# Kernel tuning notes

Hardware: AMD Instinct MI355X
Metric: run time of the kernel (lower is better)

Reference implementation:

```python
import math
import jax, jax.numpy as jnp
import numpy as np

N_TOTAL = 262144   # total objects across all groups
B = 4096           # number of groups (segments)
H = 256            # hidden_size
OS = 128           # object_size
CS = 256           # context_size


def setup_inputs() -> dict:
    key = jax.random.key(0)
    ks = jax.random.split(key, 12)
    s = 0.02
    return {
        "objects": jax.random.normal(ks[0], (N_TOTAL, OS), dtype=jnp.float32),
        "context": jax.random.normal(ks[1], (B, CS), dtype=jnp.float32),
        "segment_ids": jnp.sort(jax.random.randint(ks[2], (N_TOTAL,), 0, B, dtype=jnp.int32)),
        "num_segments": B,
        "W0": jax.random.normal(ks[3], (OS, H), dtype=jnp.float32) * s,
        "b0": jnp.zeros((H,), dtype=jnp.float32),
        "W1": jax.random.normal(ks[4], (H, H), dtype=jnp.float32) * s,
        "b1": jnp.zeros((H,), dtype=jnp.float32),
        "Wkv": jax.random.normal(ks[5], (H, 2 * H), dtype=jnp.float32) * s,
        "bkv": jnp.zeros((2 * H,), dtype=jnp.float32),
        "Wq": jax.random.normal(ks[6], (CS, H), dtype=jnp.float32) * s,
        "bq": jnp.zeros((H,), dtype=jnp.float32),
    }


def reference(objects, context, segment_ids, num_segments,
              W0, b0, W1, b1, Wkv, bkv, Wq, bq):
    # MLP over flattened objects: relu(fc0) -> relu(fc1)
    x = jax.nn.relu(objects @ W0 + b0)          # [N, H]
    x = jax.nn.relu(x @ W1 + b1)                # [N, H]
    kv = x @ Wkv + bkv                          # [N, 2H]
    k, v = kv[:, :H], kv[:, H:]                 # [N, H] each
    q = context @ Wq + bq                       # [B, H]
    q_per_obj = q[segment_ids]                  # repeat_interleave(query, split_sections)
    scale = 1.0 / math.sqrt(H)
    logits = jnp.einsum('of,of->o', q_per_obj, k) * scale  # [N]
    # per-segment stable softmax
    m = jax.ops.segment_max(logits, segment_ids, num_segments=num_segments)  # [B]
    e = jnp.exp(logits - m[segment_ids])                                     # [N]
    denom = jax.ops.segment_sum(e, segment_ids, num_segments=num_segments)   # [B]
    w = e / jnp.maximum(denom, 1e-9)[segment_ids]                            # [N]
    # per-segment weighted sum of values
    embedding = jax.ops.segment_sum(w[:, None] * v, segment_ids,
                                    num_segments=num_segments)               # [B, H]
    return embedding, w
```

## Files before the change

### kernel.cpp

```cpp
#include <hip/hip_runtime.h>
#include <hip/hip_bf16.h>


typedef __attribute__((ext_vector_type(8))) short bf16x8;
typedef __attribute__((ext_vector_type(4))) float f32x4;
typedef __attribute__((ext_vector_type(4))) short s16x4;

__device__ __forceinline__ float b2f(short s) {
    unsigned int u = ((unsigned int)(unsigned short)s) << 16;
    float f;
    __builtin_memcpy(&f, &u, 4);
    return f;
}
__device__ __forceinline__ short f2b(float x) {
    __hip_bfloat16 h = __float2bfloat16(x);
    short s;
    __builtin_memcpy(&s, &h, 2);
    return s;
}
__device__ __forceinline__ unsigned pack2(float a, float b) {
    return ((unsigned)(unsigned short)f2b(a)) | (((unsigned)(unsigned short)f2b(b)) << 16);
}
__device__ __forceinline__ f32x4 vmax0(f32x4 v) {
    f32x4 r;
    r[0] = fmaxf(v[0], 0.f); r[1] = fmaxf(v[1], 0.f);
    r[2] = fmaxf(v[2], 0.f); r[3] = fmaxf(v[3], 0.f);
    return r;
}

#define MFMA16(a, b, c) __builtin_amdgcn_mfma_f32_16x16x32_bf16(a, b, c, 0, 0, 0)
#define SWZ(row) (((row) & 7) << 4)

__global__ void kPrep0(const float* __restrict__ W0, const float* __restrict__ W1,
                       const float* __restrict__ Wkv, const float* __restrict__ Wq,
                       short* __restrict__ W0f, short* __restrict__ W1f,
                       short* __restrict__ Wkvb, short* __restrict__ Wqt) {
    int i = blockIdx.x * 256 + threadIdx.x;
    if (i < 32768) {
        int e = i & 7, lane = (i >> 3) & 63, ks = (i >> 9) & 3, mh = (i >> 11) & 3, wv = (i >> 13) & 3;
        int h = wv * 64 + mh * 16 + (lane & 15);
        int k = ks * 32 + (lane >> 4) * 8 + e;
        W0f[i] = f2b(W0[k * 256 + h]);
    }
    if (i < 65536) {
        int e = i & 7, lane = (i >> 3) & 63, ks = (i >> 9) & 7, mh = (i >> 12) & 3, wv = (i >> 14) & 3;
        int h = wv * 64 + mh * 16 + (lane & 15);
        int k = ks * 32 + (lane >> 4) * 8 + e;
        W1f[i] = f2b(W1[k * 256 + h]);
        int n = i >> 8, kk = i & 255;
        Wqt[i] = f2b(Wq[kk * 256 + n]);
    }
    if (i < 131072) Wkvb[i] = f2b(Wkv[i]);
}

__global__ __launch_bounds__(256) void kPrep1(
        const float* __restrict__ context, const short* __restrict__ Wqt,
        const float* __restrict__ bq, const short* __restrict__ Wkvb,
        const float* __restrict__ bkv, float* __restrict__ u_ws,
        float* __restrict__ c_ws) {
    __shared__ short cbuf[64 * 256];
    __shared__ float pl[4][64];
    const int t = threadIdx.x, w = t >> 6, l = t & 63;
    const int lo = l & 15, hi = l >> 4;
    const int base = blockIdx.x * 64;

    const float* src = context + (size_t)base * 256;
#pragma unroll
    for (int i = 0; i < 16; ++i) {
        int fi = (t + i * 256) * 4;
        float4 v = *(const float4*)(src + fi);
        int row = fi >> 8, col = fi & 255;
        int byte = (row << 9) + (col << 1);
        byte ^= SWZ(row);
        s16x4 pk;
        pk[0] = f2b(v.x); pk[1] = f2b(v.y); pk[2] = f2b(v.z); pk[3] = f2b(v.w);
        *(s16x4*)((char*)cbuf + byte) = pk;
    }
    __syncthreads();

    f32x4 acc[4][4] = {};
    const short* wqb = Wqt + (size_t)(w * 64 + lo) * 256 + hi * 8;
#pragma unroll
    for (int ks = 0; ks < 8; ++ks) {
        bf16x8 a[4], b[4];
#pragma unroll
        for (int m = 0; m < 4; ++m) {
            int row = m * 16 + lo;
            int byte = (row << 9) + ks * 64 + hi * 16;
            byte ^= SWZ(row);
            a[m] = *(const bf16x8*)((const char*)cbuf + byte);
        }
#pragma unroll
        for (int n = 0; n < 4; ++n) b[n] = *(const bf16x8*)(wqb + n * 16 * 256 + ks * 32);
#pragma unroll
        for (int m = 0; m < 4; ++m)
#pragma unroll
            for (int n = 0; n < 4; ++n) acc[m][n] = MFMA16(a[m], b[n], acc[m][n]);
    }
    __syncthreads();

    float bqv[4];
#pragma unroll
    for (int n = 0; n < 4; ++n) bqv[n] = bq[w * 64 + n * 16 + lo];
#pragma unroll
    for (int m = 0; m < 4; ++m)
#pragma unroll
        for (int n = 0; n < 4; ++n)
#pragma unroll
            for (int j = 0; j < 4; ++j) {
                float q = acc[m][n][j] + bqv[n];
                int row = m * 16 + hi * 4 + j;
                int col = w * 64 + n * 16 + lo;
                int byte = (row << 9) + (col << 1);
                byte ^= SWZ(row);
                *(short*)((char*)cbuf + byte) = f2b(q);
            }
    __syncthreads();

    {
        float p = 0.f;
#pragma unroll
        for (int j = 0; j < 8; ++j) {
            int col = w * 64 + j * 8;
            int byte = (l << 9) + (col << 1);
            byte ^= SWZ(l);
            bf16x8 xv = *(const bf16x8*)((const char*)cbuf + byte);
            const float* bp = bkv + col;
            p += b2f(xv[0]) * bp[0] + b2f(xv[1]) * bp[1] + b2f(xv[2]) * bp[2] + b2f(xv[3]) * bp[3]
               + b2f(xv[4]) * bp[4] + b2f(xv[5]) * bp[5] + b2f(xv[6]) * bp[6] + b2f(xv[7]) * bp[7];
        }
        pl[w][l] = p;
    }
    __syncthreads();
    if (t < 64) c_ws[base + t] = (pl[0][t] + pl[1][t] + pl[2][t] + pl[3][t]) * 0.0625f;

#pragma unroll
    for (int m = 0; m < 4; ++m)
#pragma unroll
        for (int n = 0; n < 4; ++n) acc[m][n] = (f32x4){0.f, 0.f, 0.f, 0.f};
    const short* wkb = Wkvb + (size_t)(w * 64 + lo) * 512 + hi * 8;
#pragma unroll
    for (int ks = 0; ks < 8; ++ks) {
        bf16x8 a[4], b[4];
#pragma unroll
        for (int m = 0; m < 4; ++m) {
            int row = m * 16 + lo;
            int byte = (row << 9) + ks * 64 + hi * 16;
            byte ^= SWZ(row);
            a[m] = *(const bf16x8*)((const char*)cbuf + byte);
        }
#pragma unroll
        for (int n = 0; n < 4; ++n) b[n] = *(const bf16x8*)(wkb + n * 16 * 512 + ks * 32);
#pragma unroll
        for (int m = 0; m < 4; ++m)
#pragma unroll
            for (int n = 0; n < 4; ++n) acc[m][n] = MFMA16(a[m], b[n], acc[m][n]);
    }
#pragma unroll
    for (int m = 0; m < 4; ++m)
#pragma unroll
        for (int n = 0; n < 4; ++n)
#pragma unroll
            for (int j = 0; j < 4; ++j) {
                int s = base + m * 16 + hi * 4 + j;
                int col = w * 64 + n * 16 + lo;
                u_ws[(size_t)s * 256 + col] = acc[m][n][j] * 0.0625f;
            }
}

__global__ __launch_bounds__(256, 3) void kA(
        const float* __restrict__ objects, const int* __restrict__ segids,
        const short* __restrict__ W0f, const short* __restrict__ W1f,
        const float* __restrict__ b0, const float* __restrict__ b1,
        const float* __restrict__ u_ws, const float* __restrict__ c_ws,
        float* __restrict__ e_ws, float* __restrict__ Y, float* __restrict__ D) {
    __shared__ char smem[49152];
    __shared__ float pl[4][64];
    __shared__ float e_sh[64];
    __shared__ int sid_sh[64];
    char* bufIn = smem;
    char* x1b   = smem + 16384;
    char* x2b   = smem;

    const int t = threadIdx.x, w = t >> 6, l = t & 63;
    const int lo = l & 15, hi = l >> 4;
    const int bid = (blockIdx.x & 7) * (gridDim.x >> 3) + (blockIdx.x >> 3);
    const size_t base_row = (size_t)bid * 64;

    if (t < 64) sid_sh[t] = segids[base_row + t];

    bf16x8 w0frag[4][4];
#pragma unroll
    for (int mh = 0; mh < 4; ++mh)
#pragma unroll
        for (int ks = 0; ks < 4; ++ks)
            w0frag[mh][ks] = *(const bf16x8*)(W0f + ((((w * 4 + mh) * 4 + ks) << 9) + (l << 3)));

    const float* src = objects + base_row * 128;
#pragma unroll
    for (int i = 0; i < 8; ++i) {
        int fi = (t + i * 256) * 4;
        float4 v = *(const float4*)(src + fi);
        int row = fi >> 7, col = fi & 127;
        int byte = (row << 8) + (col << 1);
        byte ^= SWZ(row);
        uint2 pk;
        pk.x = pack2(v.x, v.y);
        pk.y = pack2(v.z, v.w);
        *(uint2*)(bufIn + byte) = pk;
    }
    __syncthreads();

    f32x4 acc[4][4] = {};
#pragma unroll
    for (int ks = 0; ks < 4; ++ks) {
        bf16x8 bv[4];
#pragma unroll
        for (int nn = 0; nn < 4; ++nn) {
            int m = nn * 16 + lo;
            int byte = (m << 8) + (ks << 6) + (hi << 4);
            byte ^= SWZ(m);
            bv[nn] = *(const bf16x8*)(bufIn + byte);
        }
        __builtin_amdgcn_s_setprio(1);
#pragma unroll
        for (int mh = 0; mh < 4; ++mh)
#pragma unroll
            for (int nn = 0; nn < 4; ++nn) acc[mh][nn] = MFMA16(w0frag[mh][ks], bv[nn], acc[mh][nn]);
        __builtin_amdgcn_s_setprio(0);
    }

#pragma unroll
    for (int mh = 0; mh < 4; ++mh) {
        f32x4 bb = *(const f32x4*)(b0 + w * 64 + mh * 16 + hi * 4);
#pragma unroll
        for (int nn = 0; nn < 4; ++nn) {
            f32x4 v = vmax0(acc[mh][nn] + bb);
            int m = nn * 16 + lo;
            int byte = (m << 9) + ((w * 64 + mh * 16 + hi * 4) << 1);
            byte ^= SWZ(m);
            uint2 pk;
            pk.x = pack2(v[0], v[1]);
            pk.y = pack2(v[2], v[3]);
            *(uint2*)(x1b + byte) = pk;
        }
    }
    __syncthreads();

#pragma unroll
    for (int mh = 0; mh < 4; ++mh)
#pragma unroll
        for (int nn = 0; nn < 4; ++nn) acc[mh][nn] = (f32x4){0.f, 0.f, 0.f, 0.f};
#pragma unroll
    for (int ks = 0; ks < 8; ++ks) {
        bf16x8 av[4], bv[4];
#pragma unroll
        for (int mh = 0; mh < 4; ++mh)
            av[mh] = *(const bf16x8*)(W1f + ((((w * 4 + mh) * 8 + ks) << 9) + (l << 3)));
#pragma unroll
        for (int nn = 0; nn < 4; ++nn) {
            int m = nn * 16 + lo;
            int byte = (m << 9) + (ks << 6) + (hi << 4);
            byte ^= SWZ(m);
            bv[nn] = *(const bf16x8*)(x1b + byte);
        }
        __builtin_amdgcn_s_setprio(1);
#pragma unroll
        for (int mh = 0; mh < 4; ++mh)
#pragma unroll
            for (int nn = 0; nn < 4; ++nn) acc[mh][nn] = MFMA16(av[mh], bv[nn], acc[mh][nn]);
        __builtin_amdgcn_s_setprio(0);
    }

    int sids[4];
#pragma unroll
    for (int nn = 0; nn < 4; ++nn) sids[nn] = sid_sh[nn * 16 + lo];
    f32x4 pacc[4] = {};
#pragma unroll
    for (int mh = 0; mh < 4; ++mh) {
        f32x4 bb = *(const f32x4*)(b1 + w * 64 + mh * 16 + hi * 4);
#pragma unroll
        for (int nn = 0; nn < 4; ++nn) {
            f32x4 u4 = *(const f32x4*)(u_ws + (size_t)sids[nn] * 256 + w * 64 + mh * 16 + hi * 4);
            f32x4 v = vmax0(acc[mh][nn] + bb);
            acc[mh][nn] = v;
            pacc[nn] += v * u4;
        }
    }
#pragma unroll
    for (int nn = 0; nn < 4; ++nn) {
        float p = (pacc[nn][0] + pacc[nn][1]) + (pacc[nn][2] + pacc[nn][3]);
        p += __shfl_xor(p, 16);
        p += __shfl_xor(p, 32);
        if (hi == 0) pl[w][nn * 16 + lo] = p;
    }
    __syncthreads();

    if (t < 64) {
        float logit = pl[0][t] + pl[1][t] + pl[2][t] + pl[3][t] + c_ws[sid_sh[t]];
        float e = __expf(logit);
        e_sh[t] = e;
        e_ws[base_row + t] = e;
    }

#pragma unroll
    for (int mh = 0; mh < 4; ++mh) {
#pragma unroll
        for (int nn = 0; nn < 4; ++nn) {
            int m = nn * 16 + lo;
            int byte = (m << 9) + ((w * 64 + mh * 16 + hi * 4) << 1);
            byte ^= SWZ(m);
            uint2 pk;
            pk.x = pack2(acc[mh][nn][0], acc[mh][nn][1]);
            pk.y = pack2(acc[mh][nn][2], acc[mh][nn][3]);
            *(uint2*)(x2b + byte) = pk;
        }
    }
    __syncthreads();

    {
        float ysum = 0.f, dsum = 0.f;
#pragma unroll
        for (int r = 0; r < 64; ++r) {
            float er = e_sh[r];
            int byte = ((r << 9) + (t << 1)) ^ SWZ(r);
            ysum += er * b2f(*(const short*)(x2b + byte));
            dsum += er;
            if ((r == 63) || (sid_sh[r + 1] != sid_sh[r])) {
                int s = sid_sh[r];
                atomicAdd(Y + (size_t)s * 256 + t, ysum);
                if (t == 0) atomicAdd(D + s, dsum);
                ysum = 0.f;
                dsum = 0.f;
            }
        }
    }
}

__global__ __launch_bounds__(256) void kEmbW(const float* __restrict__ Y,
                                             const float* __restrict__ D,
                                             const float* __restrict__ Wkv,
                                             const float* __restrict__ bkv,
                                             const float* __restrict__ e,
                                             const int* __restrict__ segids,
                                             float* __restrict__ emb,
                                             float* __restrict__ wout, int nobj) {
    __shared__ float ysh[8][256];
    __shared__ float sw[8];
    const int t = threadIdx.x;
    const int s0 = blockIdx.x * 8;
#pragma unroll
    for (int i = 0; i < 8; ++i) {
        float d = D[s0 + i];
        float dm = fmaxf(d, 1e-9f);
        ysh[i][t] = Y[(size_t)(s0 + i) * 256 + t] / dm;
        if (t == 0) sw[i] = d / dm;
    }
    __syncthreads();
    float acc[8] = {0.f, 0.f, 0.f, 0.f, 0.f, 0.f, 0.f, 0.f};
    for (int h = 0; h < 256; ++h) {
        float wv = Wkv[(size_t)h * 512 + 256 + t];
#pragma unroll
        for (int i = 0; i < 8; ++i) acc[i] += ysh[i][h] * wv;
    }
    float bv = bkv[256 + t];
#pragma unroll
    for (int i = 0; i < 8; ++i) emb[(size_t)(s0 + i) * 256 + t] = acc[i] + sw[i] * bv;

    for (int i = blockIdx.x * 256 + t; i < nobj; i += gridDim.x * 256)
        wout[i] = e[i] / fmaxf(D[segids[i]], 1e-9f);
}

extern "C" void kernel_launch(void* const* d_in, const int* in_sizes, int n_in,
                              void* d_out, int out_size, void* d_ws, size_t ws_size,
                              hipStream_t stream) {
    const float* objects = (const float*)d_in[0];
    const float* context = (const float*)d_in[1];
    const int* segids    = (const int*)d_in[2];
    const float* W0  = (const float*)d_in[4];
    const float* b0  = (const float*)d_in[5];
    const float* W1  = (const float*)d_in[6];
    const float* b1  = (const float*)d_in[7];
    const float* Wkv = (const float*)d_in[8];
    const float* bkv = (const float*)d_in[9];
    const float* Wq  = (const float*)d_in[10];
    const float* bq  = (const float*)d_in[11];

    const int NT = in_sizes[2];
    const int B  = in_sizes[1] / 256;

    char* wsb = (char*)d_ws;
    short* W0f  = (short*)(wsb + 0);
    short* W1f  = (short*)(wsb + 65536);
    short* Wkvb = (short*)(wsb + 196608);
    short* Wqt  = (short*)(wsb + 458752);
    float* u_ws = (float*)(wsb + 589824);
    float* c_ws = (float*)(wsb + 4784128);
    float* e_ws = (float*)(wsb + 4800512);
    float* Y    = (float*)(wsb + 5849088);
    float* D    = (float*)(wsb + 10043392);

    float* emb_out = (float*)d_out;
    float* w_out   = (float*)d_out + (size_t)B * 256;

    hipMemsetAsync(wsb + 5849088, 0, 4194304 + 16384, stream);
    kPrep0<<<512, 256, 0, stream>>>(W0, W1, Wkv, Wq, W0f, W1f, Wkvb, Wqt);
    kPrep1<<<B / 64, 256, 0, stream>>>(context, Wqt, bq, Wkvb, bkv, u_ws, c_ws);
    kA<<<NT / 64, 256, 0, stream>>>(objects, segids, W0f, W1f, b0, b1, u_ws, c_ws, e_ws, Y, D);
    kEmbW<<<B / 8, 256, 0, stream>>>(Y, D, Wkv, bkv, e_ws, segids, emb_out, w_out, NT);
}
```

Baseline: 137.0 us.

## Split kA hidden dimension across eight waves with 512-thread blocks

Doubles the kA block from 4 to 8 waves, so each wave computes 32 hidden columns instead of 64 in both MLP layers. Per-wave accumulators and weight fragments halve, which cuts register pressure and lets more waves stay resident per CU to hide latency. The weight prepack layout and the final segment reduction are reworked to match: each half of the block reduces 32 of the 64 rows, which adds atomics at the row-32 boundary. The trade-off is more B-fragment LDS reads per MFMA and more barrier participants.

```diff
diff --git a/kernel.cpp b/kernel.cpp
--- a/kernel.cpp
+++ b/kernel.cpp
@@ -37,14 +37,14 @@
                        short* __restrict__ Wkvb, short* __restrict__ Wqt) {
     int i = blockIdx.x * 256 + threadIdx.x;
     if (i < 32768) {
-        int e = i & 7, lane = (i >> 3) & 63, ks = (i >> 9) & 3, mh = (i >> 11) & 3, wv = (i >> 13) & 3;
-        int h = wv * 64 + mh * 16 + (lane & 15);
+        int e = i & 7, lane = (i >> 3) & 63, ks = (i >> 9) & 3, wh = (i >> 11) & 15;
+        int h = wh * 16 + (lane & 15);
         int k = ks * 32 + (lane >> 4) * 8 + e;
         W0f[i] = f2b(W0[k * 256 + h]);
     }
     if (i < 65536) {
-        int e = i & 7, lane = (i >> 3) & 63, ks = (i >> 9) & 7, mh = (i >> 12) & 3, wv = (i >> 14) & 3;
-        int h = wv * 64 + mh * 16 + (lane & 15);
+        int e = i & 7, lane = (i >> 3) & 63, ks = (i >> 9) & 7, wh = (i >> 12) & 15;
+        int h = wh * 16 + (lane & 15);
         int k = ks * 32 + (lane >> 4) * 8 + e;
         W1f[i] = f2b(W1[k * 256 + h]);
         int n = i >> 8, kk = i & 255;
@@ -168,14 +168,14 @@
             }
 }
 
-__global__ __launch_bounds__(256, 3) void kA(
+__global__ __launch_bounds__(512, 4) void kA(
         const float* __restrict__ objects, const int* __restrict__ segids,
         const short* __restrict__ W0f, const short* __restrict__ W1f,
         const float* __restrict__ b0, const float* __restrict__ b1,
         const float* __restrict__ u_ws, const float* __restrict__ c_ws,
         float* __restrict__ e_ws, float* __restrict__ Y, float* __restrict__ D) {
     __shared__ char smem[49152];
-    __shared__ float pl[4][64];
+    __shared__ float pl[8][64];
     __shared__ float e_sh[64];
     __shared__ int sid_sh[64];
     char* bufIn = smem;
@@ -189,17 +189,17 @@
 
     if (t < 64) sid_sh[t] = segids[base_row + t];
 
-    bf16x8 w0frag[4][4];
-#pragma unroll
-    for (int mh = 0; mh < 4; ++mh)
+    bf16x8 w0frag[2][4];
+#pragma unroll
+    for (int mh = 0; mh < 2; ++mh)
 #pragma unroll
         for (int ks = 0; ks < 4; ++ks)
-            w0frag[mh][ks] = *(const bf16x8*)(W0f + ((((w * 4 + mh) * 4 + ks) << 9) + (l << 3)));
+            w0frag[mh][ks] = *(const bf16x8*)(W0f + ((((w * 2 + mh) * 4 + ks) << 9) + (l << 3)));
 
     const float* src = objects + base_row * 128;
 #pragma unroll
-    for (int i = 0; i < 8; ++i) {
-        int fi = (t + i * 256) * 4;
+    for (int i = 0; i < 4; ++i) {
+        int fi = (t + i * 512) * 4;
         float4 v = *(const float4*)(src + fi);
         int row = fi >> 7, col = fi & 127;
         int byte = (row << 8) + (col << 1);
@@ -211,7 +211,7 @@
     }
     __syncthreads();
 
-    f32x4 acc[4][4] = {};
+    f32x4 acc[2][4] = {};
 #pragma unroll
     for (int ks = 0; ks < 4; ++ks) {
         bf16x8 bv[4];
@@ -224,20 +224,21 @@
         }
         __builtin_amdgcn_s_setprio(1);
 #pragma unroll
-        for (int mh = 0; mh < 4; ++mh)
+        for (int mh = 0; mh < 2; ++mh)
 #pragma unroll
             for (int nn = 0; nn < 4; ++nn) acc[mh][nn] = MFMA16(w0frag[mh][ks], bv[nn], acc[mh][nn]);
         __builtin_amdgcn_s_setprio(0);
     }
 
 #pragma unroll
-    for (int mh = 0; mh < 4; ++mh) {
-        f32x4 bb = *(const f32x4*)(b0 + w * 64 + mh * 16 + hi * 4);
+    for (int mh = 0; mh < 2; ++mh) {
+        const int hcol = (w * 2 + mh) * 16 + hi * 4;
+        f32x4 bb = *(const f32x4*)(b0 + hcol);
 #pragma unroll
         for (int nn = 0; nn < 4; ++nn) {
             f32x4 v = vmax0(acc[mh][nn] + bb);
             int m = nn * 16 + lo;
-            int byte = (m << 9) + ((w * 64 + mh * 16 + hi * 4) << 1);
+            int byte = (m << 9) + (hcol << 1);
             byte ^= SWZ(m);
             uint2 pk;
             pk.x = pack2(v[0], v[1]);
@@ -248,15 +249,15 @@
     __syncthreads();
 
 #pragma unroll
-    for (int mh = 0; mh < 4; ++mh)
+    for (int mh = 0; mh < 2; ++mh)
 #pragma unroll
         for (int nn = 0; nn < 4; ++nn) acc[mh][nn] = (f32x4){0.f, 0.f, 0.f, 0.f};
 #pragma unroll
     for (int ks = 0; ks < 8; ++ks) {
-        bf16x8 av[4], bv[4];
-#pragma unroll
-        for (int mh = 0; mh < 4; ++mh)
-            av[mh] = *(const bf16x8*)(W1f + ((((w * 4 + mh) * 8 + ks) << 9) + (l << 3)));
+        bf16x8 av[2], bv[4];
+#pragma unroll
+        for (int mh = 0; mh < 2; ++mh)
+            av[mh] = *(const bf16x8*)(W1f + ((((w * 2 + mh) * 8 + ks) << 9) + (l << 3)));
 #pragma unroll
         for (int nn = 0; nn < 4; ++nn) {
             int m = nn * 16 + lo;
@@ -266,7 +267,7 @@
         }
         __builtin_amdgcn_s_setprio(1);
 #pragma unroll
-        for (int mh = 0; mh < 4; ++mh)
+        for (int mh = 0; mh < 2; ++mh)
 #pragma unroll
             for (int nn = 0; nn < 4; ++nn) acc[mh][nn] = MFMA16(av[mh], bv[nn], acc[mh][nn]);
         __builtin_amdgcn_s_setprio(0);
@@ -277,11 +278,12 @@
     for (int nn = 0; nn < 4; ++nn) sids[nn] = sid_sh[nn * 16 + lo];
     f32x4 pacc[4] = {};
 #pragma unroll
-    for (int mh = 0; mh < 4; ++mh) {
-        f32x4 bb = *(const f32x4*)(b1 + w * 64 + mh * 16 + hi * 4);
+    for (int mh = 0; mh < 2; ++mh) {
+        const int hcol = (w * 2 + mh) * 16 + hi * 4;
+        f32x4 bb = *(const f32x4*)(b1 + hcol);
 #pragma unroll
         for (int nn = 0; nn < 4; ++nn) {
-            f32x4 u4 = *(const f32x4*)(u_ws + (size_t)sids[nn] * 256 + w * 64 + mh * 16 + hi * 4);
+            f32x4 u4 = *(const f32x4*)(u_ws + (size_t)sids[nn] * 256 + hcol);
             f32x4 v = vmax0(acc[mh][nn] + bb);
             acc[mh][nn] = v;
             pacc[nn] += v * u4;
@@ -297,18 +299,20 @@
     __syncthreads();
 
     if (t < 64) {
-        float logit = pl[0][t] + pl[1][t] + pl[2][t] + pl[3][t] + c_ws[sid_sh[t]];
+        float logit = ((pl[0][t] + pl[1][t]) + (pl[2][t] + pl[3][t]))
+                    + ((pl[4][t] + pl[5][t]) + (pl[6][t] + pl[7][t])) + c_ws[sid_sh[t]];
         float e = __expf(logit);
         e_sh[t] = e;
         e_ws[base_row + t] = e;
     }
 
 #pragma unroll
-    for (int mh = 0; mh < 4; ++mh) {
+    for (int mh = 0; mh < 2; ++mh) {
+        const int hcol = (w * 2 + mh) * 16 + hi * 4;
 #pragma unroll
         for (int nn = 0; nn < 4; ++nn) {
             int m = nn * 16 + lo;
-            int byte = (m << 9) + ((w * 64 + mh * 16 + hi * 4) << 1);
+            int byte = (m << 9) + (hcol << 1);
             byte ^= SWZ(m);
             uint2 pk;
             pk.x = pack2(acc[mh][nn][0], acc[mh][nn][1]);
@@ -319,17 +323,21 @@
     __syncthreads();
 
     {
+        const int col = t & 255;
+        const int hbase = (t >> 8) * 32;
+        const int hend = hbase + 31;
         float ysum = 0.f, dsum = 0.f;
 #pragma unroll
-        for (int r = 0; r < 64; ++r) {
+        for (int rr = 0; rr < 32; ++rr) {
+            const int r = hbase + rr;
             float er = e_sh[r];
-            int byte = ((r << 9) + (t << 1)) ^ SWZ(r);
+            int byte = ((r << 9) + (col << 1)) ^ SWZ(r);
             ysum += er * b2f(*(const short*)(x2b + byte));
             dsum += er;
-            if ((r == 63) || (sid_sh[r + 1] != sid_sh[r])) {
+            if ((r == hend) || (sid_sh[r + 1] != sid_sh[r])) {
                 int s = sid_sh[r];
-                atomicAdd(Y + (size_t)s * 256 + t, ysum);
-                if (t == 0) atomicAdd(D + s, dsum);
+                atomicAdd(Y + (size_t)s * 256 + col, ysum);
+                if (col == 0) atomicAdd(D + s, dsum);
                 ysum = 0.f;
                 dsum = 0.f;
             }
@@ -406,6 +414,6 @@
     hipMemsetAsync(wsb + 5849088, 0, 4194304 + 16384, stream);
     kPrep0<<<512, 256, 0, stream>>>(W0, W1, Wkv, Wq, W0f, W1f, Wkvb, Wqt);
     kPrep1<<<B / 64, 256, 0, stream>>>(context, Wqt, bq, Wkvb, bkv, u_ws, c_ws);
-    kA<<<NT / 64, 256, 0, stream>>>(objects, segids, W0f, W1f, b0, b1, u_ws, c_ws, e_ws, Y, D);
+    kA<<<NT / 64, 512, 0, stream>>>(objects, segids, W0f, W1f, b0, b1, u_ws, c_ws, e_ws, Y, D);
     kEmbW<<<B / 8, 256, 0, stream>>>(Y, D, Wkv, bkv, e_ws, segids, emb_out, w_out, NT);
 }
```

After: 139.1 us. About the same (+1.6%).
